# Kernel optimization log

Hardware: AMD Instinct MI355X
Metric: run time of the kernel (lower is better)

The kernel has to match this reference:

```python
import jax, jax.numpy as jnp
import numpy as np

N_NODES = 50000
N_EDGES = 640000
IN_C = 128
HID = 128


def gcn_conv(x, edge_index, W, b):
    """PyG GCNConv: out = D^-1/2 (A + I) D^-1/2 (x @ W) + b, with self-loops added."""
    n = x.shape[0]
    loop = jnp.arange(n, dtype=edge_index.dtype)
    src = jnp.concatenate([edge_index[0], loop])  # [E+N]
    dst = jnp.concatenate([edge_index[1], loop])
    # degree of each node counting self-loop, computed on destination side
    deg = jax.ops.segment_sum(jnp.ones_like(dst, dtype=x.dtype), dst, num_segments=n)
    dinv = jnp.where(deg > 0, jax.lax.rsqrt(deg), 0.0)
    norm = dinv[src] * dinv[dst]  # [E+N]
    h = x @ W                      # transform first (cheaper than post-aggregation when in>=out)
    msg = h[src] * norm[:, None]   # gather + normalize  [E+N, HID]
    out = jax.ops.segment_sum(msg, dst, num_segments=n)  # scatter-add
    return out + b


def setup_inputs() -> dict:
    key = jax.random.key(0)
    ks = jax.random.split(key, 8)
    x = jax.random.normal(ks[0], (N_NODES, IN_C), dtype=jnp.float32)
    edge_index = jax.random.randint(ks[1], (2, N_EDGES), 0, N_NODES, dtype=jnp.int64)
    s_in = 1.0 / np.sqrt(IN_C)
    s_h = 1.0 / np.sqrt(HID)
    s_l = 1.0 / np.sqrt(2 * HID)
    W1 = jax.random.normal(ks[2], (IN_C, HID), dtype=jnp.float32) * s_in
    b1 = jnp.zeros((HID,), dtype=jnp.float32)
    W2 = jax.random.normal(ks[3], (HID, HID), dtype=jnp.float32) * s_h
    b2 = jnp.zeros((HID,), dtype=jnp.float32)
    Wlin = jax.random.normal(ks[4], (2 * HID, HID), dtype=jnp.float32) * s_l
    blin = jax.random.normal(ks[5], (HID,), dtype=jnp.float32) * s_l
    return {"x": x, "edge_index": edge_index, "W1": W1, "b1": b1,
            "W2": W2, "b2": b2, "Wlin": Wlin, "blin": blin}


def reference(x, edge_index, W1, b1, W2, b2, Wlin, blin):
    x1 = jax.nn.relu(gcn_conv(x, edge_index, W1, b1))
    x2 = jax.nn.relu(gcn_conv(x1, edge_index, W2, b2))
    out = jnp.concatenate([x1, x2], axis=-1) @ Wlin + blin
    return out
```

## Files before the change

kernel.cpp:

```cpp
#include <hip/hip_runtime.h>


#define THREADS 256

typedef __attribute__((ext_vector_type(8))) _Float16 half8v;
typedef __attribute__((ext_vector_type(2))) _Float16 half2v;
typedef __attribute__((ext_vector_type(4))) float f32x4;

__device__ __forceinline__ int edge_at(const int* e32, const long long* e64,
                                       int is64, long long idx) {
    return is64 ? (int)e64[idx] : e32[idx];
}

__global__ void init_kernel(const unsigned int* e, int* flag, int* cnt, int N) {
    int n = blockIdx.x * blockDim.x + threadIdx.x;
    if (n < N) cnt[n] = 0;
    if (blockIdx.x == 0 && threadIdx.x == 0) {
        int is64 = 1;
        for (int i = 1; i < 64; i += 2)
            if (e[i] != 0u) { is64 = 0; break; }
        flag[0] = is64;
        flag[1] = 0;
    }
}

__global__ void count_kernel(const int* e32, const long long* e64, const int* flag,
                             int E, int* cnt) {
    int e = blockIdx.x * blockDim.x + threadIdx.x;
    if (e >= E) return;
    int is64 = *flag;
    int d = edge_at(e32, e64, is64, (long long)E + e);
    atomicAdd(&cnt[d], 1);
}

__global__ void rowptr_kernel(const int* __restrict__ cnt, int* __restrict__ rowptr,
                              int* __restrict__ fill, float* __restrict__ dinv,
                              int* total, int N) {
    int n = blockIdx.x * blockDim.x + threadIdx.x;
    int lane = threadIdx.x & 63;
    int c = (n < N) ? cnt[n] : 0;
    if (n < N) dinv[n] = rsqrtf((float)(c + 1));
    int pre = c;
    #pragma unroll
    for (int d = 1; d < 64; d <<= 1) {
        int v = __shfl_up(pre, d);
        if (lane >= d) pre += v;
    }
    int wavesum = __shfl(pre, 63);
    int base = 0;
    if (lane == 63) base = atomicAdd(total, wavesum);
    base = __shfl(base, 63);
    int p = base + pre - c;
    if (n < N) { rowptr[n] = p; fill[n] = p; }
}

__global__ void scatter_kernel(const int* e32, const long long* e64, const int* flag,
                               int E, int* fill, int* col) {
    int e = blockIdx.x * blockDim.x + threadIdx.x;
    if (e >= E) return;
    int is64 = *flag;
    int s = edge_at(e32, e64, is64, e);
    int d = edge_at(e32, e64, is64, (long long)E + e);
    int p = atomicAdd(&fill[d], 1);
    col[p] = s;
}

__device__ __forceinline__ size_t fragidx(int k, int ncol) {
    int ks = k >> 5, fg = (k >> 3) & 3, i = k & 7;
    int n = ncol >> 4, fr = ncol & 15;
    return ((size_t)(ks * 8 + n) * 512) + (size_t)(fg * 16 + fr) * 8 + i;
}

__global__ void convw_kernel(const float* __restrict__ W1, const float* __restrict__ W2,
                             const float* __restrict__ WL,
                             _Float16* __restrict__ F1, _Float16* __restrict__ F2,
                             _Float16* __restrict__ FL) {
    int i = blockIdx.x * blockDim.x + threadIdx.x;
    if (i >= 65536) return;
    const float* W; _Float16* F; int j;
    if (i < 16384)      { W = W1; F = F1; j = i; }
    else if (i < 32768) { W = W2; F = F2; j = i - 16384; }
    else                { W = WL; F = FL; j = i - 32768; }
    int k = j >> 7, n = j & 127;
    F[fragidx(k, n)] = (_Float16)W[j];
}

__device__ __forceinline__ half8v loadA8(const _Float16* p) {
    return *(const half8v*)p;
}
__device__ __forceinline__ half8v loadA8(const float* p) {
    float4 v0 = *(const float4*)p;
    float4 v1 = *(const float4*)(p + 4);
    half8v o = {(_Float16)v0.x, (_Float16)v0.y, (_Float16)v0.z, (_Float16)v0.w,
                (_Float16)v1.x, (_Float16)v1.y, (_Float16)v1.z, (_Float16)v1.w};
    return o;
}

template <int K, typename AT, typename OT>
__global__ __launch_bounds__(256, (K > 128 ? 2 : 3)) void mgemm_kernel(
        const AT* __restrict__ A, int lda,
        const _Float16* __restrict__ Wf,
        const float* __restrict__ bias,
        OT* __restrict__ C, int ldc, int M) {
    constexpr int NK = K >> 5;
    __shared__ _Float16 ws[NK * 8 * 512];

    int tid = threadIdx.x;
    int lane = tid & 63;
    int w = tid >> 6;
    int fr = lane & 15;
    int fg = lane >> 4;
    int kb = fg * 8;
    int rowW = blockIdx.x * 128 + w * 32;

    half8v a[NK * 2];
    #pragma unroll
    for (int ks = 0; ks < NK; ++ks) {
        #pragma unroll
        for (int m = 0; m < 2; ++m) {
            int row = rowW + m * 16 + fr;
            if (row >= M) row = M - 1;
            a[ks * 2 + m] = loadA8(A + (size_t)row * lda + ks * 32 + kb);
        }
    }

    {
        constexpr int SW = K / 16;
        const uint4* src = (const uint4*)Wf;
        uint4* dst = (uint4*)ws;
        uint4 tmp[SW];
        #pragma unroll
        for (int s = 0; s < SW; ++s) tmp[s] = src[tid + 256 * s];
        #pragma unroll
        for (int s = 0; s < SW; ++s) dst[tid + 256 * s] = tmp[s];
    }
    __syncthreads();

    f32x4 acc[2][8];
    #pragma unroll
    for (int m = 0; m < 2; ++m)
        #pragma unroll
        for (int n = 0; n < 8; ++n)
            acc[m][n] = (f32x4){0.f, 0.f, 0.f, 0.f};

    #pragma unroll
    for (int ks = 0; ks < NK; ++ks) {
        #pragma unroll
        for (int n = 0; n < 8; ++n) {
            half8v bh = *(const half8v*)(ws + (size_t)(ks * 8 + n) * 512 + lane * 8);
            acc[0][n] = __builtin_amdgcn_mfma_f32_16x16x32_f16(a[ks * 2 + 0], bh, acc[0][n], 0, 0, 0);
            acc[1][n] = __builtin_amdgcn_mfma_f32_16x16x32_f16(a[ks * 2 + 1], bh, acc[1][n], 0, 0, 0);
        }
    }

    int crow = fg * 4;
    #pragma unroll
    for (int m = 0; m < 2; ++m) {
        #pragma unroll
        for (int r = 0; r < 4; ++r) {
            int row = rowW + m * 16 + crow + r;
            if (row < M) {
                #pragma unroll
                for (int n = 0; n < 8; ++n) {
                    int c = n * 16 + fr;
                    float v = acc[m][n][r];
                    if (bias) v += bias[c];
                    C[(size_t)row * ldc + c] = (OT)v;
                }
            }
        }
    }
}

__global__ __launch_bounds__(256) void agg_kernel(
        const _Float16* __restrict__ h, const int* __restrict__ rowptr,
        const int* __restrict__ cnt, const int* __restrict__ col,
        const float* __restrict__ dinv, const float* __restrict__ bias,
        _Float16* __restrict__ out, int ldo, int N) {
    int node = blockIdx.x * 4 + (threadIdx.x >> 6);
    if (node >= N) return;
    int lane = threadIdx.x & 63;

    float di = dinv[node];
    float wself = di * di;
    half2v v = ((const half2v*)(h + (size_t)node * 128))[lane];
    float ax0 = (float)v[0] * wself, ay0 = (float)v[1] * wself;
    float ax1 = 0.f, ay1 = 0.f, ax2 = 0.f, ay2 = 0.f, ax3 = 0.f, ay3 = 0.f;

    int p = rowptr[node];
    int en = p + cnt[node];
    for (; p + 3 < en; p += 4) {
        int s0 = col[p], s1 = col[p + 1], s2 = col[p + 2], s3 = col[p + 3];
        float w0 = dinv[s0] * di, w1 = dinv[s1] * di;
        float w2 = dinv[s2] * di, w3 = dinv[s3] * di;
        half2v h0 = ((const half2v*)(h + (size_t)s0 * 128))[lane];
        half2v h1 = ((const half2v*)(h + (size_t)s1 * 128))[lane];
        half2v h2 = ((const half2v*)(h + (size_t)s2 * 128))[lane];
        half2v h3 = ((const half2v*)(h + (size_t)s3 * 128))[lane];
        ax0 += (float)h0[0] * w0; ay0 += (float)h0[1] * w0;
        ax1 += (float)h1[0] * w1; ay1 += (float)h1[1] * w1;
        ax2 += (float)h2[0] * w2; ay2 += (float)h2[1] * w2;
        ax3 += (float)h3[0] * w3; ay3 += (float)h3[1] * w3;
    }
    for (; p < en; ++p) {
        int s0 = col[p];
        float w0 = dinv[s0] * di;
        half2v h0 = ((const half2v*)(h + (size_t)s0 * 128))[lane];
        ax0 += (float)h0[0] * w0; ay0 += (float)h0[1] * w0;
    }
    float ax = (ax0 + ax1) + (ax2 + ax3) + bias[2 * lane];
    float ay = (ay0 + ay1) + (ay2 + ay3) + bias[2 * lane + 1];
    ax = fmaxf(ax, 0.f);
    ay = fmaxf(ay, 0.f);
    half2v o = {(_Float16)ax, (_Float16)ay};
    ((half2v*)(out + (size_t)node * ldo))[lane] = o;
}

extern "C" void kernel_launch(void* const* d_in, const int* in_sizes, int n_in,
                              void* d_out, int out_size, void* d_ws, size_t ws_size,
                              hipStream_t stream) {
    const float* x    = (const float*)d_in[0];
    const void*  edges = d_in[1];
    const float* W1   = (const float*)d_in[2];
    const float* b1   = (const float*)d_in[3];
    const float* W2   = (const float*)d_in[4];
    const float* b2   = (const float*)d_in[5];
    const float* Wlin = (const float*)d_in[6];
    const float* blin = (const float*)d_in[7];
    float* out = (float*)d_out;

    const int C = 128;
    int N = in_sizes[0] / C;
    int E = in_sizes[1] / 2;

    char* w = (char*)d_ws;
    auto carve = [&](size_t bytes) {
        char* p = w;
        w += (bytes + 255) & ~(size_t)255;
        return (void*)p;
    };
    int*   flag   = (int*)carve(256);
    int*   cnt    = (int*)carve((size_t)N * 4);
    int*   rowptr = (int*)carve((size_t)N * 4);
    int*   fill   = (int*)carve((size_t)N * 4);
    float* dinv   = (float*)carve((size_t)N * 4);
    int*   col    = (int*)carve((size_t)E * 4);
    _Float16* h   = (_Float16*)carve((size_t)N * 128 * 2);
    _Float16* xc  = (_Float16*)carve((size_t)N * 256 * 2);
    _Float16* F1  = (_Float16*)carve((size_t)128 * 128 * 2);
    _Float16* F2  = (_Float16*)carve((size_t)128 * 128 * 2);
    _Float16* FL  = (_Float16*)carve((size_t)256 * 128 * 2);

    const int* e32 = (const int*)edges;
    const long long* e64 = (const long long*)edges;

    init_kernel<<<(N + THREADS - 1) / THREADS, THREADS, 0, stream>>>(
        (const unsigned int*)edges, flag, cnt, N);
    count_kernel<<<(E + THREADS - 1) / THREADS, THREADS, 0, stream>>>(e32, e64, flag, E, cnt);
    rowptr_kernel<<<(N + THREADS - 1) / THREADS, THREADS, 0, stream>>>(
        cnt, rowptr, fill, dinv, flag + 1, N);
    scatter_kernel<<<(E + THREADS - 1) / THREADS, THREADS, 0, stream>>>(
        e32, e64, flag, E, fill, col);
    convw_kernel<<<(65536 + THREADS - 1) / THREADS, THREADS, 0, stream>>>(
        W1, W2, Wlin, F1, F2, FL);

    int gemm_grid = (N + 127) / 128;
    int agg_grid  = (N + 3) / 4;

    mgemm_kernel<128, float, _Float16><<<gemm_grid, 256, 0, stream>>>(
        x, 128, F1, nullptr, h, 128, N);
    agg_kernel<<<agg_grid, 256, 0, stream>>>(h, rowptr, cnt, col, dinv, b1, xc, 256, N);
    mgemm_kernel<128, _Float16, _Float16><<<gemm_grid, 256, 0, stream>>>(
        xc, 256, F2, nullptr, h, 128, N);
    agg_kernel<<<agg_grid, 256, 0, stream>>>(h, rowptr, cnt, col, dinv, b2, xc + 128, 256, N);
    mgemm_kernel<256, _Float16, float><<<gemm_grid, 256, 0, stream>>>(
        xc, 256, FL, blin, out, 128, N);
}
```

Before: 274.0 us.

## Build CSR with LDS-chunked counting fused into first GEMM launch

Replaces the global-atomic count/scatter CSR build with a chunked scheme. Edges are split into 64 chunks and nodes into 4 ranges, with per-block counts kept in LDS atomics. A per-node prefix over chunks then gives deterministic-offset placement, also done with LDS atomics. The counting blocks share a launch with the first GEMM so the two overlap. Init and weight conversion merge into one prep kernel, cutting launch count and global atomic contention at the cost of extra passes over the edge list and a 64xN counts buffer.

```diff
diff --git a/kernel.cpp b/kernel.cpp
--- a/kernel.cpp
+++ b/kernel.cpp
@@ -2,7 +2,11 @@
 
 
 #define THREADS 256
-
+#define NCHUNK 64
+#define RN     12544
+#define CPAD   50176
+
+typedef unsigned int uint;
 typedef __attribute__((ext_vector_type(8))) _Float16 half8v;
 typedef __attribute__((ext_vector_type(2))) _Float16 half2v;
 typedef __attribute__((ext_vector_type(4))) float f32x4;
@@ -10,59 +14,6 @@
 __device__ __forceinline__ int edge_at(const int* e32, const long long* e64,
                                        int is64, long long idx) {
     return is64 ? (int)e64[idx] : e32[idx];
-}
-
-__global__ void init_kernel(const unsigned int* e, int* flag, int* cnt, int N) {
-    int n = blockIdx.x * blockDim.x + threadIdx.x;
-    if (n < N) cnt[n] = 0;
-    if (blockIdx.x == 0 && threadIdx.x == 0) {
-        int is64 = 1;
-        for (int i = 1; i < 64; i += 2)
-            if (e[i] != 0u) { is64 = 0; break; }
-        flag[0] = is64;
-        flag[1] = 0;
-    }
-}
-
-__global__ void count_kernel(const int* e32, const long long* e64, const int* flag,
-                             int E, int* cnt) {
-    int e = blockIdx.x * blockDim.x + threadIdx.x;
-    if (e >= E) return;
-    int is64 = *flag;
-    int d = edge_at(e32, e64, is64, (long long)E + e);
-    atomicAdd(&cnt[d], 1);
-}
-
-__global__ void rowptr_kernel(const int* __restrict__ cnt, int* __restrict__ rowptr,
-                              int* __restrict__ fill, float* __restrict__ dinv,
-                              int* total, int N) {
-    int n = blockIdx.x * blockDim.x + threadIdx.x;
-    int lane = threadIdx.x & 63;
-    int c = (n < N) ? cnt[n] : 0;
-    if (n < N) dinv[n] = rsqrtf((float)(c + 1));
-    int pre = c;
-    #pragma unroll
-    for (int d = 1; d < 64; d <<= 1) {
-        int v = __shfl_up(pre, d);
-        if (lane >= d) pre += v;
-    }
-    int wavesum = __shfl(pre, 63);
-    int base = 0;
-    if (lane == 63) base = atomicAdd(total, wavesum);
-    base = __shfl(base, 63);
-    int p = base + pre - c;
-    if (n < N) { rowptr[n] = p; fill[n] = p; }
-}
-
-__global__ void scatter_kernel(const int* e32, const long long* e64, const int* flag,
-                               int E, int* fill, int* col) {
-    int e = blockIdx.x * blockDim.x + threadIdx.x;
-    if (e >= E) return;
-    int is64 = *flag;
-    int s = edge_at(e32, e64, is64, e);
-    int d = edge_at(e32, e64, is64, (long long)E + e);
-    int p = atomicAdd(&fill[d], 1);
-    col[p] = s;
 }
 
 __device__ __forceinline__ size_t fragidx(int k, int ncol) {
@@ -71,18 +22,26 @@
     return ((size_t)(ks * 8 + n) * 512) + (size_t)(fg * 16 + fr) * 8 + i;
 }
 
-__global__ void convw_kernel(const float* __restrict__ W1, const float* __restrict__ W2,
-                             const float* __restrict__ WL,
-                             _Float16* __restrict__ F1, _Float16* __restrict__ F2,
-                             _Float16* __restrict__ FL) {
+__global__ void prep_kernel(const unsigned int* e, int* flag,
+                            const float* __restrict__ W1, const float* __restrict__ W2,
+                            const float* __restrict__ WL,
+                            _Float16* __restrict__ F1, _Float16* __restrict__ F2,
+                            _Float16* __restrict__ FL) {
     int i = blockIdx.x * blockDim.x + threadIdx.x;
-    if (i >= 65536) return;
-    const float* W; _Float16* F; int j;
-    if (i < 16384)      { W = W1; F = F1; j = i; }
-    else if (i < 32768) { W = W2; F = F2; j = i - 16384; }
-    else                { W = WL; F = FL; j = i - 32768; }
-    int k = j >> 7, n = j & 127;
-    F[fragidx(k, n)] = (_Float16)W[j];
+    if (i == 0) flag[1] = 0;
+    if (blockIdx.x == 0 && threadIdx.x < 64) {
+        unsigned int v = (threadIdx.x < 32) ? e[2 * threadIdx.x + 1] : 0u;
+        unsigned long long b = __ballot(v != 0u);
+        if (threadIdx.x == 0) flag[0] = (b == 0ull) ? 1 : 0;
+    }
+    if (i < 65536) {
+        const float* W; _Float16* F; int j;
+        if (i < 16384)      { W = W1; F = F1; j = i; }
+        else if (i < 32768) { W = W2; F = F2; j = i - 16384; }
+        else                { W = WL; F = FL; j = i - 32768; }
+        int k = j >> 7, n = j & 127;
+        F[fragidx(k, n)] = (_Float16)W[j];
+    }
 }
 
 __device__ __forceinline__ half8v loadA8(const _Float16* p) {
@@ -97,21 +56,20 @@
 }
 
 template <int K, typename AT, typename OT>
-__global__ __launch_bounds__(256, (K > 128 ? 2 : 3)) void mgemm_kernel(
+__device__ __forceinline__ void mgemm_body(
+        int bid, _Float16* ws,
         const AT* __restrict__ A, int lda,
         const _Float16* __restrict__ Wf,
         const float* __restrict__ bias,
         OT* __restrict__ C, int ldc, int M) {
     constexpr int NK = K >> 5;
-    __shared__ _Float16 ws[NK * 8 * 512];
-
     int tid = threadIdx.x;
     int lane = tid & 63;
     int w = tid >> 6;
     int fr = lane & 15;
     int fg = lane >> 4;
     int kb = fg * 8;
-    int rowW = blockIdx.x * 128 + w * 32;
+    int rowW = bid * 128 + w * 32;
 
     half8v a[NK * 2];
     #pragma unroll
@@ -123,7 +81,6 @@
             a[ks * 2 + m] = loadA8(A + (size_t)row * lda + ks * 32 + kb);
         }
     }
-
     {
         constexpr int SW = K / 16;
         const uint4* src = (const uint4*)Wf;
@@ -168,6 +125,113 @@
                     C[(size_t)row * ldc + c] = (OT)v;
                 }
             }
+        }
+    }
+}
+
+template <int K, typename AT, typename OT>
+__global__ __launch_bounds__(256, (K > 128 ? 2 : 3)) void mgemm_kernel(
+        const AT* __restrict__ A, int lda,
+        const _Float16* __restrict__ Wf, const float* __restrict__ bias,
+        OT* __restrict__ C, int ldc, int M) {
+    constexpr int NK = K >> 5;
+    __shared__ _Float16 ws[NK * 8 * 512];
+    mgemm_body<K, AT, OT>(blockIdx.x, ws, A, lda, Wf, bias, C, ldc, M);
+}
+
+__device__ __forceinline__ void count_body(
+        int abid, uint* lcnt,
+        const int* e32, const long long* e64, const int* flag,
+        int E, int* counts, int N) {
+    int chunk = abid >> 2, range = abid & 3;
+    int nbase = range * RN;
+    int rn = N - nbase; if (rn > RN) rn = RN;
+    int tid = threadIdx.x;
+    for (int i = tid; i < RN; i += THREADS) lcnt[i] = 0u;
+    __syncthreads();
+    int is64 = flag[0];
+    int CH = (E + NCHUNK - 1) / NCHUNK;
+    int e0 = chunk * CH;
+    int e1 = e0 + CH; if (e1 > E) e1 = E;
+    for (int i = e0 + tid; i < e1; i += THREADS) {
+        int d = edge_at(e32, e64, is64, (long long)E + i);
+        uint r = (uint)(d - nbase);
+        if (r < (uint)rn) atomicAdd(&lcnt[r], 1u);
+    }
+    __syncthreads();
+    for (int i = tid; i < rn; i += THREADS)
+        counts[(size_t)chunk * CPAD + nbase + i] = (int)lcnt[i];
+}
+
+__global__ __launch_bounds__(256, 3) void mgemm_count_kernel(
+        const float* __restrict__ A, const _Float16* __restrict__ Wf,
+        _Float16* __restrict__ C, int M, int GB,
+        const int* e32, const long long* e64, const int* flag,
+        int E, int* counts, int N) {
+    __shared__ alignas(16) unsigned char shbuf[RN * 4];
+    int bid = blockIdx.x;
+    if (bid < GB) {
+        mgemm_body<128, float, _Float16>(bid, (_Float16*)shbuf, A, 128, Wf,
+                                         nullptr, C, 128, M);
+    } else {
+        count_body(bid - GB, (uint*)shbuf, e32, e64, flag, E, counts, N);
+    }
+}
+
+__global__ void prefix_kernel(int* __restrict__ counts, int* __restrict__ rowptr,
+                              int* __restrict__ cnt, float* __restrict__ dinv,
+                              int* cursor, int N) {
+    int n = blockIdx.x * blockDim.x + threadIdx.x;
+    int lane = threadIdx.x & 63;
+    int s = 0;
+    if (n < N) {
+        #pragma unroll 4
+        for (int c = 0; c < NCHUNK; ++c) {
+            size_t idx = (size_t)c * CPAD + n;
+            int v = counts[idx];
+            counts[idx] = s;
+            s += v;
+        }
+        cnt[n] = s;
+        dinv[n] = rsqrtf((float)(s + 1));
+    }
+    int pre = s;
+    #pragma unroll
+    for (int d = 1; d < 64; d <<= 1) {
+        int v = __shfl_up(pre, d);
+        if (lane >= d) pre += v;
+    }
+    int wavesum = __shfl(pre, 63);
+    int base = 0;
+    if (lane == 63) base = atomicAdd(cursor, wavesum);
+    base = __shfl(base, 63);
+    if (n < N) rowptr[n] = base + pre - s;
+}
+
+__global__ __launch_bounds__(256, 3) void place_kernel(
+        const int* e32, const long long* e64, const int* flag, int E,
+        const int* __restrict__ counts, const int* __restrict__ rowptr,
+        int* __restrict__ col, int N) {
+    __shared__ uint lptr[RN];
+    int abid = blockIdx.x;
+    int chunk = abid >> 2, range = abid & 3;
+    int nbase = range * RN;
+    int rn = N - nbase; if (rn > RN) rn = RN;
+    int tid = threadIdx.x;
+    for (int i = tid; i < rn; i += THREADS)
+        lptr[i] = (uint)(counts[(size_t)chunk * CPAD + nbase + i] + rowptr[nbase + i]);
+    __syncthreads();
+    int is64 = flag[0];
+    int CH = (E + NCHUNK - 1) / NCHUNK;
+    int e0 = chunk * CH;
+    int e1 = e0 + CH; if (e1 > E) e1 = E;
+    for (int i = e0 + tid; i < e1; i += THREADS) {
+        int d = edge_at(e32, e64, is64, (long long)E + i);
+        uint r = (uint)(d - nbase);
+        if (r < (uint)rn) {
+            int s = edge_at(e32, e64, is64, i);
+            uint slot = atomicAdd(&lptr[r], 1u);
+            col[slot] = s;
         }
     }
 }
@@ -242,8 +306,8 @@
     int*   flag   = (int*)carve(256);
     int*   cnt    = (int*)carve((size_t)N * 4);
     int*   rowptr = (int*)carve((size_t)N * 4);
-    int*   fill   = (int*)carve((size_t)N * 4);
     float* dinv   = (float*)carve((size_t)N * 4);
+    int*   counts = (int*)carve((size_t)NCHUNK * CPAD * 4);
     int*   col    = (int*)carve((size_t)E * 4);
     _Float16* h   = (_Float16*)carve((size_t)N * 128 * 2);
     _Float16* xc  = (_Float16*)carve((size_t)N * 256 * 2);
@@ -254,21 +318,22 @@
     const int* e32 = (const int*)edges;
     const long long* e64 = (const long long*)edges;
 
-    init_kernel<<<(N + THREADS - 1) / THREADS, THREADS, 0, stream>>>(
-        (const unsigned int*)edges, flag, cnt, N);
-    count_kernel<<<(E + THREADS - 1) / THREADS, THREADS, 0, stream>>>(e32, e64, flag, E, cnt);
-    rowptr_kernel<<<(N + THREADS - 1) / THREADS, THREADS, 0, stream>>>(
-        cnt, rowptr, fill, dinv, flag + 1, N);
-    scatter_kernel<<<(E + THREADS - 1) / THREADS, THREADS, 0, stream>>>(
-        e32, e64, flag, E, fill, col);
-    convw_kernel<<<(65536 + THREADS - 1) / THREADS, THREADS, 0, stream>>>(
-        W1, W2, Wlin, F1, F2, FL);
-
     int gemm_grid = (N + 127) / 128;
+    int abc_grid  = NCHUNK * 4;
     int agg_grid  = (N + 3) / 4;
 
-    mgemm_kernel<128, float, _Float16><<<gemm_grid, 256, 0, stream>>>(
-        x, 128, F1, nullptr, h, 128, N);
+    prep_kernel<<<256, THREADS, 0, stream>>>(
+        (const unsigned int*)edges, flag, W1, W2, Wlin, F1, F2, FL);
+
+    mgemm_count_kernel<<<gemm_grid + abc_grid, THREADS, 0, stream>>>(
+        x, F1, h, N, gemm_grid, e32, e64, flag, E, counts, N);
+
+    prefix_kernel<<<(N + THREADS - 1) / THREADS, THREADS, 0, stream>>>(
+        counts, rowptr, cnt, dinv, flag + 1, N);
+
+    place_kernel<<<abc_grid, THREADS, 0, stream>>>(
+        e32, e64, flag, E, counts, rowptr, col, N);
+
     agg_kernel<<<agg_grid, 256, 0, stream>>>(h, rowptr, cnt, col, dinv, b1, xc, 256, N);
     mgemm_kernel<128, _Float16, _Float16><<<gemm_grid, 256, 0, stream>>>(
         xc, 256, F2, nullptr, h, 128, N);
```

Measured after the change: 248.7 us. 1.1x faster.
